# Kernel optimization log

Hardware: AMD Instinct MI355X
Metric: run time of the kernel (lower is better)

Reference implementation:

```python
import jax, jax.numpy as jnp
import numpy as np

N_GRAPHS = 2048
EPS = 1e-5


def _segment_mean(x, seg, num_segments):
    s = jax.ops.segment_sum(x, seg, num_segments=num_segments)
    cnt = jax.ops.segment_sum(jnp.ones((x.shape[0], 1), x.dtype), seg, num_segments=num_segments)
    return s / jnp.maximum(cnt, 1.0)


def _deepset(x, seg, gw, gb, lw):
    # xm = scatter_mean(x, batch); out = Gamma(x) - Lambda(xm)[batch]
    xm = _segment_mean(x, seg, N_GRAPHS)
    return x @ gw.T + gb - (xm @ lw.T)[seg]


def _batchnorm(x, g, b):
    mu = jnp.mean(x, axis=0)
    var = jnp.mean((x - mu) ** 2, axis=0)  # biased var, as torch BN training fwd
    return (x - mu) * jax.lax.rsqrt(var + EPS) * g + b


def setup_inputs() -> dict:
    key = jax.random.key(0)
    ks = jax.random.split(key, 12)
    N, F, H, P = 500000, 128, 128, 8
    in0 = F + 2 * P  # 144
    x = jax.random.normal(ks[0], (N, F), jnp.float32)
    batch = jnp.sort(jax.random.randint(ks[1], (N,), 0, N_GRAPHS))
    pers0 = jax.random.normal(ks[2], (P, N, 2), jnp.float32)
    s = lambda k, sh: jax.random.normal(k, sh, jnp.float32) * 0.05
    return {
        "x": x, "batch": batch, "pers0": pers0,
        "g1w": s(ks[3], (H, in0)), "g1b": s(ks[4], (H,)), "l1w": s(ks[5], (H, in0)),
        "g2w": s(ks[6], (F, H)), "g2b": s(ks[7], (F,)), "l2w": s(ks[8], (F, H)),
        "bn_g": jnp.ones((F,), jnp.float32), "bn_b": jnp.zeros((F,), jnp.float32),
    }


def reference(x, batch, pers0, g1w, g1b, l1w, g2w, g2b, l2w, bn_g, bn_b):
    N = x.shape[0]
    # cat([x, pers0.permute(1,0,2).reshape(N, -1)], 1)
    x0 = jnp.concatenate([x, jnp.transpose(pers0, (1, 0, 2)).reshape(N, -1)], axis=1)
    x0 = jax.nn.relu(_deepset(x0, batch, g1w, g1b, l1w))
    x0 = _deepset(x0, batch, g2w, g2b, l2w)
    return x + _batchnorm(x0, bn_g, bn_b)
```

## Files before the change

kernel.cpp:

```cpp
#include <hip/hip_runtime.h>

typedef float    f32x4  __attribute__((ext_vector_type(4)));
typedef __bf16   bf16x8 __attribute__((ext_vector_type(8)));
typedef unsigned short us4 __attribute__((ext_vector_type(4)));
typedef unsigned short us8 __attribute__((ext_vector_type(8)));

#define NGRAPHS 2048
#define K1DIM 144
#define K1PAD 160
#define NREP  32

static __device__ __forceinline__ unsigned short f2bf(float f) {
    __bf16 h = (__bf16)f;
    return __builtin_bit_cast(unsigned short, h);
}
static __device__ __forceinline__ float bf2f(unsigned short u) {
    __bf16 h = __builtin_bit_cast(__bf16, u);
    return (float)h;
}

__global__ void k_prep(const float* __restrict__ g1w, const float* __restrict__ g2w,
                       unsigned short* __restrict__ W1, unsigned short* __restrict__ W2) {
    int n = blockIdx.x;
    int t = threadIdx.x;
    if (t < K1PAD) W1[n * K1PAD + t] = (t < K1DIM) ? f2bf(g1w[n * K1DIM + t]) : (unsigned short)0;
    if (t < 128)   W2[n * 128 + t]   = f2bf(g2w[n * 128 + t]);
}

__global__ void k_seg1(const float* __restrict__ x, const float* __restrict__ pers,
                       const int* __restrict__ batch, float* __restrict__ sum1,
                       float* __restrict__ cnt, int N) {
    int t  = threadIdx.x;
    int r0 = blockIdx.x * 256;
    if (r0 >= N) return;
    int rend   = min(r0 + 256, N);
    bool activ = (t < K1DIM);
    int   cur = batch[r0];
    float acc = 0.f;
    int   runlen = 0;
    for (int r = r0; r < rend; ++r) {
        int s = batch[r];
        if (s != cur) {
            if (activ) atomicAdd(&sum1[(size_t)cur * K1DIM + t], acc);
            if (t == 0) atomicAdd(&cnt[cur], (float)runlen);
            acc = 0.f; runlen = 0; cur = s;
        }
        float v = 0.f;
        if (t < 128) {
            v = x[(size_t)r * 128 + t];
        } else if (t < K1DIM) {
            int q = t - 128, p = q >> 1, c = q & 1;
            v = pers[(size_t)p * 2 * (size_t)N + (size_t)r * 2 + c];
        }
        acc += v; runlen++;
    }
    if (activ) atomicAdd(&sum1[(size_t)cur * K1DIM + t], acc);
    if (t == 0) atomicAdd(&cnt[cur], (float)runlen);
}

__global__ void k_corr(const float* __restrict__ sums, const float* __restrict__ cnt,
                       const float* __restrict__ lw, const float* __restrict__ gb,
                       float* __restrict__ cp, int K) {
    int g = blockIdx.x, n = threadIdx.x;
    float inv = 1.f / fmaxf(cnt[g], 1.f);
    const float* srow = sums + (size_t)g * K;
    const float* wrow = lw   + (size_t)n * K;
    float acc = 0.f;
    for (int k = 0; k < K; ++k) acc += srow[k] * wrow[k];
    cp[(size_t)g * 128 + n] = gb[n] - acc * inv;
}

__global__ __launch_bounds__(256, 4) void k_gemm1(
        const float* __restrict__ x, const float* __restrict__ pers,
        const int* __restrict__ batch, const unsigned short* __restrict__ W1,
        const float* __restrict__ c1p, unsigned short* __restrict__ x1,
        float* __restrict__ sum2, int N) {
    int tid  = threadIdx.x;
    int wave = tid >> 6, lane = tid & 63;
    int m = lane & 15, quad = lane >> 4;
    long tileBase = (long)blockIdx.x * 64 + wave * 16;
    if (tileBase >= N) return;

    long arow = tileBase + m;
    if (arow > (long)N - 1) arow = (long)N - 1;
    const float* xr = x + (size_t)arow * 128;

    bf16x8 a[5];
    #pragma unroll
    for (int kb = 0; kb < 4; ++kb) {
        float4 u0 = *(const float4*)(xr + kb * 32 + quad * 8);
        float4 u1 = *(const float4*)(xr + kb * 32 + quad * 8 + 4);
        bf16x8 t;
        t[0] = (__bf16)u0.x; t[1] = (__bf16)u0.y; t[2] = (__bf16)u0.z; t[3] = (__bf16)u0.w;
        t[4] = (__bf16)u1.x; t[5] = (__bf16)u1.y; t[6] = (__bf16)u1.z; t[7] = (__bf16)u1.w;
        a[kb] = t;
    }
    {
        bf16x8 t;
        #pragma unroll
        for (int j = 0; j < 8; ++j) t[j] = (__bf16)0.f;
        if (quad < 2) {
            #pragma unroll
            for (int pp = 0; pp < 4; ++pp) {
                int p = quad * 4 + pp;
                float2 v = *(const float2*)(pers + (size_t)p * 2 * (size_t)N + (size_t)arow * 2);
                t[pp * 2]     = (__bf16)v.x;
                t[pp * 2 + 1] = (__bf16)v.y;
            }
        }
        a[4] = t;
    }

    f32x4 acc[8];
    #pragma unroll
    for (int nt = 0; nt < 8; ++nt) acc[nt] = (f32x4){0.f, 0.f, 0.f, 0.f};

    #pragma unroll
    for (int kb = 0; kb < 5; ++kb) {
        #pragma unroll
        for (int nt = 0; nt < 8; ++nt) {
            bf16x8 b = *(const bf16x8*)(W1 + (size_t)(nt * 16 + m) * K1PAD + kb * 32 + quad * 8);
            acc[nt] = __builtin_amdgcn_mfma_f32_16x16x32_bf16(a[kb], b, acc[nt], 0, 0, 0);
        }
    }

    int segr[4];
    #pragma unroll
    for (int r = 0; r < 4; ++r) {
        long grow = tileBase + quad * 4 + r;
        if (grow >= N) { segr[r] = -1; continue; }
        int seg = batch[grow];
        segr[r] = seg;
        const float* crow = c1p + (size_t)seg * 128;
        #pragma unroll
        for (int nt = 0; nt < 8; ++nt) {
            int n = nt * 16 + m;
            float v = fmaxf(acc[nt][r] + crow[n], 0.f);
            acc[nt][r] = v;
            x1[(size_t)grow * 128 + n] = f2bf(v);
        }
    }

    long lastRow = tileBase + 15; if (lastRow > (long)N - 1) lastRow = (long)N - 1;
    int sLo = batch[tileBase];
    int sHi = batch[lastRow];
    for (int sg = sLo; sg <= sHi; ++sg) {
        #pragma unroll
        for (int nt = 0; nt < 8; ++nt) {
            float p = 0.f;
            #pragma unroll
            for (int r = 0; r < 4; ++r) p += (segr[r] == sg) ? acc[nt][r] : 0.f;
            p += __shfl_xor(p, 16);
            p += __shfl_xor(p, 32);
            if (quad == 0) atomicAdd(&sum2[(size_t)sg * 128 + nt * 16 + m], p);
        }
    }
}

__global__ __launch_bounds__(256) void k_gemm2(
        const unsigned short* __restrict__ x1, const int* __restrict__ batch,
        const unsigned short* __restrict__ W2, const float* __restrict__ c2p,
        float* __restrict__ x2f, unsigned short* __restrict__ x2b, int mode,
        float* __restrict__ bnp, int N) {
    __shared__ float lsum[128], lsq[128];
    int tid = threadIdx.x;
    if (tid < 128) { lsum[tid] = 0.f; lsq[tid] = 0.f; }
    __syncthreads();

    int wave = tid >> 6, lane = tid & 63;
    int m = lane & 15, quad = lane >> 4;
    long waveBase = (long)blockIdx.x * 128 + wave * 32;

    bf16x8 a[2][4];
    #pragma unroll
    for (int t = 0; t < 2; ++t) {
        long ra = waveBase + t * 16 + m;
        if (ra > (long)N - 1) ra = (long)N - 1;
        #pragma unroll
        for (int kb = 0; kb < 4; ++kb)
            a[t][kb] = *(const bf16x8*)(x1 + (size_t)ra * 128 + kb * 32 + quad * 8);
    }

    f32x4 acc[2][8];
    #pragma unroll
    for (int t = 0; t < 2; ++t)
        #pragma unroll
        for (int nt = 0; nt < 8; ++nt) acc[t][nt] = (f32x4){0.f, 0.f, 0.f, 0.f};

    #pragma unroll
    for (int nt = 0; nt < 8; ++nt) {
        #pragma unroll
        for (int kb = 0; kb < 4; ++kb) {
            bf16x8 b = *(const bf16x8*)(W2 + (size_t)(nt * 16 + m) * 128 + kb * 32 + quad * 8);
            acc[0][nt] = __builtin_amdgcn_mfma_f32_16x16x32_bf16(a[0][kb], b, acc[0][nt], 0, 0, 0);
            acc[1][nt] = __builtin_amdgcn_mfma_f32_16x16x32_bf16(a[1][kb], b, acc[1][nt], 0, 0, 0);
        }
    }

    float sumv[8], sqv[8];
    #pragma unroll
    for (int nt = 0; nt < 8; ++nt) { sumv[nt] = 0.f; sqv[nt] = 0.f; }
    #pragma unroll
    for (int t = 0; t < 2; ++t) {
        #pragma unroll
        for (int r = 0; r < 4; ++r) {
            long grow = waveBase + t * 16 + quad * 4 + r;
            bool ok = (grow < N);
            int seg = ok ? batch[grow] : 0;
            const float* crow = c2p + (size_t)seg * 128;
            #pragma unroll
            for (int nt = 0; nt < 8; ++nt) {
                int n = nt * 16 + m;
                float v = acc[t][nt][r] + crow[n];
                if (ok) {
                    if (mode) x2b[(size_t)grow * 128 + n] = f2bf(v);
                    else      x2f[(size_t)grow * 128 + n] = v;
                    sumv[nt] += v;
                    sqv[nt]  += v * v;
                }
            }
        }
    }
    #pragma unroll
    for (int nt = 0; nt < 8; ++nt) {
        float s = sumv[nt], q = sqv[nt];
        s += __shfl_xor(s, 16); s += __shfl_xor(s, 32);
        q += __shfl_xor(q, 16); q += __shfl_xor(q, 32);
        if (quad == 0) {
            atomicAdd(&lsum[nt * 16 + m], s);
            atomicAdd(&lsq[nt * 16 + m], q);
        }
    }
    __syncthreads();
    if (tid < 128) {
        int rep = (int)(blockIdx.x & (NREP - 1));
        atomicAdd(&bnp[rep * 256 + tid],       lsum[tid]);
        atomicAdd(&bnp[rep * 256 + 128 + tid], lsq[tid]);
    }
}

__global__ void k_bnfin(const float* __restrict__ bnp, const float* __restrict__ bn_g,
                        const float* __restrict__ bn_b, float* __restrict__ bnscale,
                        float* __restrict__ bnshift, int N) {
    int t = threadIdx.x;
    float s = 0.f, q = 0.f;
    for (int rep = 0; rep < NREP; ++rep) {
        s += bnp[rep * 256 + t];
        q += bnp[rep * 256 + 128 + t];
    }
    float invN = 1.f / (float)N;
    float mu  = s * invN;
    float var = fmaxf(q * invN - mu * mu, 0.f);
    float sc  = bn_g[t] * rsqrtf(var + 1e-5f);
    bnscale[t] = sc;
    bnshift[t] = bn_b[t] - mu * sc;
}

__global__ void k_final(const float* __restrict__ x, const unsigned short* __restrict__ x2b,
                        const float* __restrict__ x2f, int mode,
                        const float* __restrict__ bnscale, const float* __restrict__ bnshift,
                        float* __restrict__ out, long nThreads) {
    long i = (long)blockIdx.x * blockDim.x + threadIdx.x;
    if (i >= nThreads) return;
    long base = i * 8;
    int n0 = (int)(base & 127);
    float4 sc0 = *(const float4*)(bnscale + n0);
    float4 sc1 = *(const float4*)(bnscale + n0 + 4);
    float4 sh0 = *(const float4*)(bnshift + n0);
    float4 sh1 = *(const float4*)(bnshift + n0 + 4);
    float4 xa = *(const float4*)(x + base);
    float4 xb = *(const float4*)(x + base + 4);
    float v[8];
    if (mode) {
        us8 u = *(const us8*)(x2b + base);
        #pragma unroll
        for (int j = 0; j < 8; ++j) v[j] = bf2f(u[j]);
    } else {
        float4 va = *(const float4*)(x2f + base);
        float4 vb = *(const float4*)(x2f + base + 4);
        v[0] = va.x; v[1] = va.y; v[2] = va.z; v[3] = va.w;
        v[4] = vb.x; v[5] = vb.y; v[6] = vb.z; v[7] = vb.w;
    }
    float4 oa, ob;
    oa.x = xa.x + v[0] * sc0.x + sh0.x;
    oa.y = xa.y + v[1] * sc0.y + sh0.y;
    oa.z = xa.z + v[2] * sc0.z + sh0.z;
    oa.w = xa.w + v[3] * sc0.w + sh0.w;
    ob.x = xb.x + v[4] * sc1.x + sh1.x;
    ob.y = xb.y + v[5] * sc1.y + sh1.y;
    ob.z = xb.z + v[6] * sc1.z + sh1.z;
    ob.w = xb.w + v[7] * sc1.w + sh1.w;
    *(float4*)(out + base)     = oa;
    *(float4*)(out + base + 4) = ob;
}

extern "C" void kernel_launch(void* const* d_in, const int* in_sizes, int n_in,
                              void* d_out, int out_size, void* d_ws, size_t ws_size,
                              hipStream_t stream) {
    const float* x    = (const float*)d_in[0];
    const int*   bat  = (const int*)  d_in[1];
    const float* pers = (const float*)d_in[2];
    const float* g1w  = (const float*)d_in[3];
    const float* g1b  = (const float*)d_in[4];
    const float* l1w  = (const float*)d_in[5];
    const float* g2w  = (const float*)d_in[6];
    const float* g2b  = (const float*)d_in[7];
    const float* l2w  = (const float*)d_in[8];
    const float* bng  = (const float*)d_in[9];
    const float* bnb  = (const float*)d_in[10];
    int N = in_sizes[1];
    float* out = (float*)d_out;

    char* ws = (char*)d_ws;
    float* sum1 = (float*)(ws + 0);
    float* cnt  = (float*)(ws + 1179648);
    float* sum2 = (float*)(ws + 1187840);
    float* bnp  = (float*)(ws + 2236416);
    size_t zero_bytes = 2269184;
    float* c1p  = (float*)(ws + 2269184);
    float* c2p  = (float*)(ws + 3317760);
    unsigned short* W1 = (unsigned short*)(ws + 4366336);
    unsigned short* W2 = (unsigned short*)(ws + 4407296);
    float* bnscale = (float*)(ws + 4440064);
    float* bnshift = (float*)(ws + 4440576);
    unsigned short* x1 = (unsigned short*)(ws + 4441088);
    unsigned short* x2b = (unsigned short*)(ws + 132441088);
    size_t need_bf16 = 132441088 + (size_t)N * 128 * 2;
    int mode = (ws_size >= need_bf16) ? 1 : 0;

    hipMemsetAsync(ws, 0, zero_bytes, stream);

    int gridRows256 = (N + 255) / 256;
    int gridRows64  = (N + 63) / 64;
    int gridRows128 = (N + 127) / 128;

    k_prep <<<128, 192, 0, stream>>>(g1w, g2w, W1, W2);
    k_seg1 <<<gridRows256, 192, 0, stream>>>(x, pers, bat, sum1, cnt, N);
    k_corr <<<NGRAPHS, 128, 0, stream>>>(sum1, cnt, l1w, g1b, c1p, K1DIM);
    k_gemm1<<<gridRows64, 256, 0, stream>>>(x, pers, bat, W1, c1p, x1, sum2, N);
    k_corr <<<NGRAPHS, 128, 0, stream>>>(sum2, cnt, l2w, g2b, c2p, 128);
    k_gemm2<<<gridRows128, 256, 0, stream>>>(x1, bat, W2, c2p, out, x2b, mode, bnp, N);
    k_bnfin<<<1, 128, 0, stream>>>(bnp, bng, bnb, bnscale, bnshift, N);
    long nThreads = ((long)N * 128) / 8;
    k_final<<<(int)((nThreads + 255) / 256), 256, 0, stream>>>(x, x2b, out, mode,
                                                               bnscale, bnshift, out, nThreads);
}
```

Baseline: 1.080 ms.

## Compute segment bounds by binary search and reduce first segment sum per graph

```diff
diff --git a/kernel.cpp b/kernel.cpp
--- a/kernel.cpp
+++ b/kernel.cpp
@@ -17,6 +17,18 @@
 static __device__ __forceinline__ float bf2f(unsigned short u) {
     __bf16 h = __builtin_bit_cast(__bf16, u);
     return (float)h;
+}
+
+__global__ void k_bounds(const int* __restrict__ batch, int* __restrict__ start, int N) {
+    int g = blockIdx.x * blockDim.x + threadIdx.x;
+    if (g > NGRAPHS) return;
+    if (g == NGRAPHS) { start[g] = N; return; }
+    int lo = 0, hi = N;
+    while (lo < hi) {
+        int mid = (lo + hi) >> 1;
+        if (batch[mid] < g) lo = mid + 1; else hi = mid;
+    }
+    start[g] = lo;
 }
 
 __global__ void k_prep(const float* __restrict__ g1w, const float* __restrict__ g2w,
@@ -27,35 +39,42 @@
     if (t < 128)   W2[n * 128 + t]   = f2bf(g2w[n * 128 + t]);
 }
 
-__global__ void k_seg1(const float* __restrict__ x, const float* __restrict__ pers,
-                       const int* __restrict__ batch, float* __restrict__ sum1,
-                       float* __restrict__ cnt, int N) {
-    int t  = threadIdx.x;
-    int r0 = blockIdx.x * 256;
-    if (r0 >= N) return;
-    int rend   = min(r0 + 256, N);
-    bool activ = (t < K1DIM);
-    int   cur = batch[r0];
-    float acc = 0.f;
-    int   runlen = 0;
-    for (int r = r0; r < rend; ++r) {
-        int s = batch[r];
-        if (s != cur) {
-            if (activ) atomicAdd(&sum1[(size_t)cur * K1DIM + t], acc);
-            if (t == 0) atomicAdd(&cnt[cur], (float)runlen);
-            acc = 0.f; runlen = 0; cur = s;
-        }
-        float v = 0.f;
-        if (t < 128) {
-            v = x[(size_t)r * 128 + t];
-        } else if (t < K1DIM) {
-            int q = t - 128, p = q >> 1, c = q & 1;
-            v = pers[(size_t)p * 2 * (size_t)N + (size_t)r * 2 + c];
-        }
-        acc += v; runlen++;
-    }
-    if (activ) atomicAdd(&sum1[(size_t)cur * K1DIM + t], acc);
-    if (t == 0) atomicAdd(&cnt[cur], (float)runlen);
+__global__ __launch_bounds__(256) void k_seg1(
+        const float* __restrict__ x, const float* __restrict__ pers,
+        const int* __restrict__ start, float* __restrict__ sum1,
+        float* __restrict__ cnt, int N) {
+    __shared__ f32x4 red[7][36];
+    int g = blockIdx.x;
+    int s = start[g], e = start[g + 1];
+    int tid = threadIdx.x;
+    int cg = tid % 36, rs = tid / 36;
+    f32x4 acc = {0.f, 0.f, 0.f, 0.f};
+    if (rs < 7) {
+        if (cg < 32) {
+            for (int r = s + rs; r < e; r += 7) {
+                f32x4 v = *(const f32x4*)(x + (size_t)r * 128 + cg * 4);
+                acc += v;
+            }
+        } else {
+            int j = cg - 32;
+            const float* p0 = pers + (size_t)(2 * j)     * 2 * (size_t)N;
+            const float* p1 = pers + (size_t)(2 * j + 1) * 2 * (size_t)N;
+            for (int r = s + rs; r < e; r += 7) {
+                float2 a = *(const float2*)(p0 + (size_t)r * 2);
+                float2 b = *(const float2*)(p1 + (size_t)r * 2);
+                acc[0] += a.x; acc[1] += a.y; acc[2] += b.x; acc[3] += b.y;
+            }
+        }
+        red[rs][cg] = acc;
+    }
+    __syncthreads();
+    if (tid < 36) {
+        f32x4 t = red[0][tid];
+        #pragma unroll
+        for (int k = 1; k < 7; ++k) t += red[k][tid];
+        *(f32x4*)(sum1 + (size_t)g * K1DIM + tid * 4) = t;
+    }
+    if (tid == 0) cnt[g] = (float)(e - s);
 }
 
 __global__ void k_corr(const float* __restrict__ sums, const float* __restrict__ cnt,
@@ -312,30 +331,31 @@
     float* out = (float*)d_out;
 
     char* ws = (char*)d_ws;
-    float* sum1 = (float*)(ws + 0);
-    float* cnt  = (float*)(ws + 1179648);
-    float* sum2 = (float*)(ws + 1187840);
-    float* bnp  = (float*)(ws + 2236416);
-    size_t zero_bytes = 2269184;
-    float* c1p  = (float*)(ws + 2269184);
-    float* c2p  = (float*)(ws + 3317760);
-    unsigned short* W1 = (unsigned short*)(ws + 4366336);
-    unsigned short* W2 = (unsigned short*)(ws + 4407296);
-    float* bnscale = (float*)(ws + 4440064);
-    float* bnshift = (float*)(ws + 4440576);
-    unsigned short* x1 = (unsigned short*)(ws + 4441088);
-    unsigned short* x2b = (unsigned short*)(ws + 132441088);
-    size_t need_bf16 = 132441088 + (size_t)N * 128 * 2;
+    float* sum2 = (float*)(ws + 0);
+    float* bnp  = (float*)(ws + 1048576);
+    size_t zero_bytes = 1081344;
+    int*   start = (int*)(ws + 1081344);
+    float* cnt  = (float*)(ws + 1090048);
+    float* sum1 = (float*)(ws + 1098240);
+    float* c1p  = (float*)(ws + 2277888);
+    float* c2p  = (float*)(ws + 3326464);
+    unsigned short* W1 = (unsigned short*)(ws + 4375040);
+    unsigned short* W2 = (unsigned short*)(ws + 4416000);
+    float* bnscale = (float*)(ws + 4448768);
+    float* bnshift = (float*)(ws + 4449280);
+    unsigned short* x1 = (unsigned short*)(ws + 4449792);
+    unsigned short* x2b = (unsigned short*)(ws + 132449792);
+    size_t need_bf16 = 132449792 + (size_t)N * 128 * 2;
     int mode = (ws_size >= need_bf16) ? 1 : 0;
 
     hipMemsetAsync(ws, 0, zero_bytes, stream);
 
-    int gridRows256 = (N + 255) / 256;
     int gridRows64  = (N + 63) / 64;
     int gridRows128 = (N + 127) / 128;
 
+    k_bounds<<<(NGRAPHS + 256) / 256 + 1, 256, 0, stream>>>(bat, start, N);
     k_prep <<<128, 192, 0, stream>>>(g1w, g2w, W1, W2);
-    k_seg1 <<<gridRows256, 192, 0, stream>>>(x, pers, bat, sum1, cnt, N);
+    k_seg1 <<<NGRAPHS, 256, 0, stream>>>(x, pers, start, sum1, cnt, N);
     k_corr <<<NGRAPHS, 128, 0, stream>>>(sum1, cnt, l1w, g1b, c1p, K1DIM);
     k_gemm1<<<gridRows64, 256, 0, stream>>>(x, pers, bat, W1, c1p, x1, sum2, N);
     k_corr <<<NGRAPHS, 128, 0, stream>>>(sum2, cnt, l2w, g2b, c2p, 128);
```

Result: faster. 1.018 ms (-5.8%).
